# Performance work log

Measured on AMD Instinct MI355X. Metric: run time of the kernel, lower is better.

## Reference

```python
import jax, jax.numpy as jnp
import numpy as np

N, E, F, H, L, G, O = 100000, 1600000, 128, 128, 4, 512, 10
BN_EPS = 1e-5


def setup_inputs() -> dict:
    key = jax.random.key(0)
    ks = jax.random.split(key, 12)
    x = jax.random.normal(ks[0], (N, F), dtype=jnp.float32)
    edge_index = jax.random.randint(ks[1], (2, E), 0, N, dtype=jnp.int32)
    batch = jnp.sort(jax.random.randint(ks[2], (N,), 0, G, dtype=jnp.int32))
    s = 1.0 / np.sqrt(H)
    # 4 GIN layers, input_dim == hidden_dim so params stack uniformly
    W1s = jax.random.uniform(ks[3], (L, F, H), jnp.float32, -s, s)
    b1s = jnp.zeros((L, H), jnp.float32)
    W2s = jax.random.uniform(ks[4], (L, H, H), jnp.float32, -s, s)
    b2s = jnp.zeros((L, H), jnp.float32)
    eps = jnp.zeros((L,), jnp.float32)  # learnable eps, init 0
    gammas = jnp.ones((L, H), jnp.float32)
    betas = jnp.zeros((L, H), jnp.float32)
    Din = F + L * H  # concatenated graph embedding dim
    so = 1.0 / np.sqrt(Din)
    Wout = jax.random.uniform(ks[5], (Din, O), jnp.float32, -so, so)
    bout = jnp.zeros((O,), jnp.float32)
    return {"x": x, "edge_index": edge_index, "batch": batch,
            "W1s": W1s, "b1s": b1s, "W2s": W2s, "b2s": b2s, "eps": eps,
            "gammas": gammas, "betas": betas, "Wout": Wout, "bout": bout}


def reference(x, edge_index, batch, W1s, b1s, W2s, b2s, eps, gammas, betas, Wout, bout):
    src, dst = edge_index[0], edge_index[1]
    n = x.shape[0]
    pooled = [jax.ops.segment_sum(x, batch, num_segments=G)]  # [G, F]
    h = x
    for l in range(W1s.shape[0]):
        # GINConv: MLP((1+eps)*h + sum_{j in N(i)} h_j)
        agg = jax.ops.segment_sum(h[src], dst, num_segments=n)  # [N, H]
        z = (1.0 + eps[l]) * h + agg
        z = jax.nn.relu(z @ W1s[l] + b1s[l]) @ W2s[l] + b2s[l]
        # BatchNorm1d (batch statistics, biased variance) + ReLU; dropout=identity (eval)
        mu = z.mean(axis=0)
        var = z.var(axis=0)
        z = (z - mu) * jax.lax.rsqrt(var + BN_EPS) * gammas[l] + betas[l]
        h = jax.nn.relu(z)
        pooled.append(jax.ops.segment_sum(h, batch, num_segments=G))  # [G, H]
    emb = jnp.concatenate(pooled, axis=1)  # [G, F + L*H]
    return emb @ Wout + bout  # [G, O]
```

## Files before the change

### kernel.cpp

```cpp
#include <hip/hip_runtime.h>
#include <hip/hip_bf16.h>

typedef __attribute__((ext_vector_type(8))) __bf16 bf16x8;
typedef __attribute__((ext_vector_type(4))) float f32x4;
typedef unsigned short u16;
typedef unsigned int u32;

constexpr int Nn = 100000;
constexpr int Ee = 1600000;
constexpr int Hd = 128;
constexpr int Ll = 4;
constexpr int Gg = 512;
constexpr int Oo = 10;
constexpr int Din = Hd + Ll * Hd;
constexpr int SPLIT = 8;
constexpr int NBLK = (Nn + 127) / 128;

constexpr int NB = 256;
constexpr int NPB = 392;
constexpr int BCAP = 8192;
constexpr int BATCH = 8192;
constexpr int NBATCH = (Ee + BATCH - 1) / BATCH;

__device__ __forceinline__ int swzb(int row, int bc) {
  return (row << 8) + (bc ^ ((row & 7) << 4));
}

__device__ __forceinline__ u16 f2bf(float f) {
  __hip_bfloat16 b = __float2bfloat16(f);
  u16 u;
  __builtin_memcpy(&u, &b, 2);
  return u;
}

__device__ __forceinline__ float bf2f(u32 u) { return __uint_as_float(u << 16); }

__device__ __forceinline__ int lower_bound_dev(const int* a, int n, int key) {
  int lo = 0, hi = n;
  while (lo < hi) { int mid = (lo + hi) >> 1; if (a[mid] < key) lo = mid + 1; else hi = mid; }
  return lo;
}

__global__ __launch_bounds__(256) void xcvt_kernel(const float* __restrict__ x, __hip_bfloat16* __restrict__ xb) {
  int i = blockIdx.x * 256 + threadIdx.x;
  const int total = Nn * Hd / 8;
  if (i >= total) return;
  f32x4 v0 = *(const f32x4*)(x + (size_t)i * 8);
  f32x4 v1 = *(const f32x4*)(x + (size_t)i * 8 + 4);
  uint4 o;
  o.x = (u32)f2bf(v0[0]) | ((u32)f2bf(v0[1]) << 16);
  o.y = (u32)f2bf(v0[2]) | ((u32)f2bf(v0[3]) << 16);
  o.z = (u32)f2bf(v1[0]) | ((u32)f2bf(v1[1]) << 16);
  o.w = (u32)f2bf(v1[2]) | ((u32)f2bf(v1[3]) << 16);
  *(uint4*)((u16*)xb + (size_t)i * 8) = o;
}

__global__ __launch_bounds__(256) void wprep_kernel(const float* __restrict__ W1s,
                                                    const float* __restrict__ W2s,
                                                    __hip_bfloat16* __restrict__ wt) {
  int idx = blockIdx.x * 256 + threadIdx.x;
  if (idx >= Ll * 2 * Hd * Hd) return;
  int l = idx >> 15;
  int w = (idx >> 14) & 1;
  int nn = (idx >> 7) & 127;
  int k = idx & 127;
  const float* W = w ? W2s : W1s;
  wt[idx] = __float2bfloat16(W[l * Hd * Hd + k * Hd + nn]);
}

__global__ void initgptr_kernel(int* __restrict__ gptr) {
  int i = threadIdx.x;
  if (i < NB) gptr[i] = i * BCAP;
}

__global__ __launch_bounds__(256) void binA_kernel(const int* __restrict__ src, const int* __restrict__ dst,
                                                   int* __restrict__ gptr, u32* __restrict__ buckets) {
  __shared__ int hist[NB];
  __shared__ int lbase[NB];
  __shared__ int lpos[NB];
  __shared__ int gbaseS[NB];
  __shared__ int scanT[NB];
  __shared__ u32 reorder[BATCH];
  const int tid = threadIdx.x;
  const int e0 = blockIdx.x * BATCH;
  const int n = min(BATCH, Ee - e0);

  hist[tid] = 0;
  __syncthreads();
  for (int k = tid; k < n; k += 256) {
    int d = dst[e0 + k];
    atomicAdd(&hist[d / NPB], 1);
  }
  __syncthreads();
  int v = hist[tid];
  scanT[tid] = v;
  __syncthreads();
  for (int off = 1; off < NB; off <<= 1) {
    int x = (tid >= off) ? scanT[tid - off] : 0;
    __syncthreads();
    scanT[tid] += x;
    __syncthreads();
  }
  lbase[tid] = scanT[tid] - v;
  lpos[tid] = 0;
  __syncthreads();
  for (int k = tid; k < n; k += 256) {
    int d = dst[e0 + k];
    int s = src[e0 + k];
    int b = d / NPB;
    int dlo = d - b * NPB;
    int p = lbase[b] + atomicAdd(&lpos[b], 1);
    reorder[p] = ((u32)dlo << 17) | (u32)s;
  }
  __syncthreads();
  if (hist[tid] > 0) gbaseS[tid] = atomicAdd(&gptr[tid], hist[tid]);
  __syncthreads();
  for (int p = tid; p < n; p += 256) {
    int lo = 0, hi = NB - 1;
    while (lo < hi) { int mid = (lo + hi + 1) >> 1; if (lbase[mid] <= p) lo = mid; else hi = mid - 1; }
    buckets[gbaseS[lo] + (p - lbase[lo])] = reorder[p];
  }
}

__global__ __launch_bounds__(256) void bucketscan_kernel(const int* __restrict__ gptr,
                                                         int* __restrict__ bmeta,
                                                         int* __restrict__ indptr) {
  __shared__ int sc[NB];
  int tid = threadIdx.x;
  int cnt = gptr[tid] - tid * BCAP;
  sc[tid] = cnt;
  __syncthreads();
  for (int off = 1; off < NB; off <<= 1) {
    int x = (tid >= off) ? sc[tid - off] : 0;
    __syncthreads();
    sc[tid] += x;
    __syncthreads();
  }
  bmeta[tid] = cnt;
  bmeta[NB + tid] = sc[tid] - cnt;
  if (tid == 0) indptr[Nn] = Ee;
}

__global__ __launch_bounds__(512) void place_kernel(const u32* __restrict__ buckets,
                                                    const int* __restrict__ bmeta,
                                                    int* __restrict__ indptr, int* __restrict__ adj) {
  __shared__ int ncnt[512];
  __shared__ int nofs[NPB];
  __shared__ int lcur[NPB];
  const int tid = threadIdx.x;
  const int b = blockIdx.x;
  const int cnt = bmeta[b];
  const int adjbase = bmeta[NB + b];
  const int ebase = b * BCAP;
  const int node0 = b * NPB;
  const int nnodes = min(NPB, Nn - node0);

  ncnt[tid] = 0;
  if (tid < NPB) lcur[tid] = 0;
  __syncthreads();
  for (int k = tid; k < cnt; k += 512) atomicAdd(&ncnt[buckets[ebase + k] >> 17], 1);
  __syncthreads();
  int v = ncnt[tid];
  for (int off = 1; off < 512; off <<= 1) {
    int x = (tid >= off) ? ncnt[tid - off] : 0;
    __syncthreads();
    ncnt[tid] += x;
    __syncthreads();
  }
  if (tid < NPB) nofs[tid] = ncnt[tid] - v;
  __syncthreads();
  if (tid < nnodes) indptr[node0 + tid] = adjbase + nofs[tid];
  for (int k = tid; k < cnt; k += 512) {
    u32 u = buckets[ebase + k];
    int dlo = u >> 17;
    int s = (int)(u & 0x1FFFFu);
    int p = atomicAdd(&lcur[dlo], 1);
    adj[adjbase + nofs[dlo] + p] = s;
  }
}

__global__ __launch_bounds__(256) void agg_kernel(const __hip_bfloat16* __restrict__ hb,
                                                  const int* __restrict__ indptr,
                                                  const int* __restrict__ adj,
                                                  const float* __restrict__ epsp,
                                                  int layer, __hip_bfloat16* __restrict__ t) {
  int wid = blockIdx.x * 4 + (threadIdx.x >> 6);
  if (wid >= Nn) return;
  int lane = threadIdx.x & 63;
  int cb = lane * 2;
  const u16* hp = (const u16*)hb;
  u32 selfu = *(const u32*)(hp + (size_t)wid * Hd + cb);
  float eps1 = 1.0f + epsp[layer];
  int s = __builtin_amdgcn_readfirstlane(indptr[wid]);
  int e = __builtin_amdgcn_readfirstlane(indptr[wid + 1]);
  float a0 = 0.f, a1 = 0.f;
  int p = s;
  while (p + 16 <= e) {
    u32 v[16];
    #pragma unroll
    for (int j = 0; j < 16; ++j) v[j] = *(const u32*)(hp + (size_t)adj[p + j] * Hd + cb);
    #pragma unroll
    for (int j = 0; j < 16; ++j) { a0 += bf2f(v[j] & 0xffffu); a1 += bf2f(v[j] >> 16); }
    p += 16;
  }
  if (p + 8 <= e) {
    u32 v[8];
    #pragma unroll
    for (int j = 0; j < 8; ++j) v[j] = *(const u32*)(hp + (size_t)adj[p + j] * Hd + cb);
    #pragma unroll
    for (int j = 0; j < 8; ++j) { a0 += bf2f(v[j] & 0xffffu); a1 += bf2f(v[j] >> 16); }
    p += 8;
  }
  if (p + 4 <= e) {
    u32 v[4];
    #pragma unroll
    for (int j = 0; j < 4; ++j) v[j] = *(const u32*)(hp + (size_t)adj[p + j] * Hd + cb);
    #pragma unroll
    for (int j = 0; j < 4; ++j) { a0 += bf2f(v[j] & 0xffffu); a1 += bf2f(v[j] >> 16); }
    p += 4;
  }
  for (; p < e; ++p) {
    u32 v0 = *(const u32*)(hp + (size_t)adj[p] * Hd + cb);
    a0 += bf2f(v0 & 0xffffu);
    a1 += bf2f(v0 >> 16);
  }
  a0 += eps1 * bf2f(selfu & 0xffffu);
  a1 += eps1 * bf2f(selfu >> 16);
  u32 outv = (u32)f2bf(a0) | ((u32)f2bf(a1) << 16);
  *(u32*)((u16*)t + (size_t)wid * Hd + cb) = outv;
}

__global__ __launch_bounds__(256) void mlp_kernel(const __hip_bfloat16* __restrict__ t,
                                                  const __hip_bfloat16* __restrict__ w1t,
                                                  const __hip_bfloat16* __restrict__ w2t,
                                                  const float* __restrict__ b1,
                                                  const float* __restrict__ b2,
                                                  __hip_bfloat16* __restrict__ z,
                                                  float* __restrict__ pstats) {
  __shared__ __align__(16) unsigned char sA[32 * 1024];
  __shared__ __align__(16) unsigned char sW[32 * 1024];
  const int tid = threadIdx.x;
  const int m0 = blockIdx.x * 128;

  for (int c = tid; c < 2048; c += 256) {
    int row = c >> 4, bc = (c & 15) << 4;
    int so = swzb(row, bc);
    *(uint4*)(sW + so) = *(const uint4*)((const unsigned char*)w1t + row * 256 + bc);
    uint4 av = make_uint4(0u, 0u, 0u, 0u);
    int gr = m0 + row;
    if (gr < Nn) av = *(const uint4*)((const unsigned char*)t + (size_t)gr * 256 + bc);
    *(uint4*)(sA + so) = av;
  }
  __syncthreads();

  const int lane = tid & 63;
  const int wave = tid >> 6;
  const int lrow = lane & 15;
  const int lkb = (lane >> 4) << 4;
  const int wm = wave * 32;
  const int crow = (lane >> 4) << 2;

  f32x4 acc[2][8];
  #pragma unroll
  for (int a = 0; a < 2; ++a) {
    #pragma unroll
    for (int b = 0; b < 8; ++b) acc[a][b] = (f32x4){0.f, 0.f, 0.f, 0.f};
  }

  #pragma unroll
  for (int kk = 0; kk < 4; ++kk) {
    const int kb2 = kk * 64 + lkb;
    bf16x8 a0 = *(const bf16x8*)(sA + swzb(wm + lrow, kb2));
    bf16x8 a1 = *(const bf16x8*)(sA + swzb(wm + 16 + lrow, kb2));
    #pragma unroll
    for (int nf = 0; nf < 8; ++nf) {
      bf16x8 bfr = *(const bf16x8*)(sW + swzb(nf * 16 + lrow, kb2));
      acc[0][nf] = __builtin_amdgcn_mfma_f32_16x16x32_bf16(a0, bfr, acc[0][nf], 0, 0, 0);
      acc[1][nf] = __builtin_amdgcn_mfma_f32_16x16x32_bf16(a1, bfr, acc[1][nf], 0, 0, 0);
    }
  }
  __syncthreads();

  for (int c = tid; c < 2048; c += 256) {
    int row = c >> 4, bc = (c & 15) << 4;
    *(uint4*)(sW + swzb(row, bc)) = *(const uint4*)((const unsigned char*)w2t + row * 256 + bc);
  }
  #pragma unroll
  for (int nf = 0; nf < 8; ++nf) {
    const int col = nf * 16 + lrow;
    const float bb = b1[col];
    #pragma unroll
    for (int mf = 0; mf < 2; ++mf) {
      #pragma unroll
      for (int j = 0; j < 4; ++j) {
        float v = acc[mf][nf][j] + bb;
        v = v > 0.f ? v : 0.f;
        int row = wm + mf * 16 + crow + j;
        *(u16*)(sA + swzb(row, col * 2)) = f2bf(v);
      }
    }
  }
  __syncthreads();

  f32x4 acc2[2][8];
  #pragma unroll
  for (int a = 0; a < 2; ++a) {
    #pragma unroll
    for (int b = 0; b < 8; ++b) acc2[a][b] = (f32x4){0.f, 0.f, 0.f, 0.f};
  }
  #pragma unroll
  for (int kk = 0; kk < 4; ++kk) {
    const int kb2 = kk * 64 + lkb;
    bf16x8 a0 = *(const bf16x8*)(sA + swzb(wm + lrow, kb2));
    bf16x8 a1 = *(const bf16x8*)(sA + swzb(wm + 16 + lrow, kb2));
    #pragma unroll
    for (int nf = 0; nf < 8; ++nf) {
      bf16x8 bfr = *(const bf16x8*)(sW + swzb(nf * 16 + lrow, kb2));
      acc2[0][nf] = __builtin_amdgcn_mfma_f32_16x16x32_bf16(a0, bfr, acc2[0][nf], 0, 0, 0);
      acc2[1][nf] = __builtin_amdgcn_mfma_f32_16x16x32_bf16(a1, bfr, acc2[1][nf], 0, 0, 0);
    }
  }
  __syncthreads();

  float* sred = (float*)sA;
  float* qred = (float*)(sA + 2048);
  u16* zp = (u16*)z;
  #pragma unroll
  for (int nf = 0; nf < 8; ++nf) {
    const int col = nf * 16 + lrow;
    const float bb = b2[col];
    float s = 0.f, q = 0.f;
    #pragma unroll
    for (int mf = 0; mf < 2; ++mf) {
      #pragma unroll
      for (int j = 0; j < 4; ++j) {
        int grow = m0 + wm + mf * 16 + crow + j;
        if (grow < Nn) {
          float v = acc2[mf][nf][j] + bb;
          zp[(size_t)grow * Hd + col] = f2bf(v);
          s += v; q += v * v;
        }
      }
    }
    s += __shfl_xor(s, 16, 64); s += __shfl_xor(s, 32, 64);
    q += __shfl_xor(q, 16, 64); q += __shfl_xor(q, 32, 64);
    if (lane < 16) { sred[wave * 128 + col] = s; qred[wave * 128 + col] = q; }
  }
  __syncthreads();
  if (tid < 128) {
    float a = sred[tid] + sred[128 + tid] + sred[256 + tid] + sred[384 + tid];
    pstats[(size_t)blockIdx.x * 256 + tid] = a;
  } else {
    int c = tid - 128;
    float a = qred[c] + qred[128 + c] + qred[256 + c] + qred[384 + c];
    pstats[(size_t)blockIdx.x * 256 + tid] = a;
  }
}

__global__ __launch_bounds__(256) void stats_bn_kernel(const float* __restrict__ pstats,
                                                       const float* __restrict__ gammas,
                                                       const float* __restrict__ betas,
                                                       int layer, float* __restrict__ ss) {
  __shared__ float reds[256];
  __shared__ float redq[256];
  int f = blockIdx.x;
  int t = threadIdx.x;
  float s = 0.f, q = 0.f;
  for (int i = t; i < NBLK; i += 256) {
    s += pstats[(size_t)i * 256 + f];
    q += pstats[(size_t)i * 256 + 128 + f];
  }
  reds[t] = s; redq[t] = q;
  __syncthreads();
  for (int o = 128; o > 0; o >>= 1) {
    if (t < o) { reds[t] += reds[t + o]; redq[t] += redq[t + o]; }
    __syncthreads();
  }
  if (t == 0) {
    const float invn = 1.0f / (float)Nn;
    float mu = reds[0] * invn;
    float var = redq[0] * invn - mu * mu;
    float sc = gammas[layer * Hd + f] * rsqrtf(var + 1e-5f);
    ss[f] = sc;
    ss[Hd + f] = betas[layer * Hd + f] - mu * sc;
  }
}

__global__ __launch_bounds__(128) void pool_kernel(const __hip_bfloat16* __restrict__ v,
                                                   const int* __restrict__ batch,
                                                   float* __restrict__ emb, int colOff) {
  int g = blockIdx.x / SPLIT, sp = blockIdx.x % SPLIT;
  int c2 = (threadIdx.x & 63) * 2;
  int rh = threadIdx.x >> 6;
  int lo = lower_bound_dev(batch, Nn, g);
  int hi = lower_bound_dev(batch, Nn, g + 1);
  int len = hi - lo;
  if (len <= 0) return;
  int chunk = (len + SPLIT - 1) / SPLIT;
  int rs = lo + sp * chunk;
  int re = min(rs + chunk, hi);
  if (rs >= re) return;
  const u16* vp = (const u16*)v;
  float a0 = 0.f, a1 = 0.f;
  for (int i = rs + rh; i < re; i += 2) {
    u32 u = *(const u32*)(vp + (size_t)i * Hd + c2);
    a0 += bf2f(u & 0xffffu);
    a1 += bf2f(u >> 16);
  }
  atomicAdd(&emb[g * Din + colOff + c2], a0);
  atomicAdd(&emb[g * Din + colOff + c2 + 1], a1);
}

__global__ __launch_bounds__(128) void bn_pool_kernel(const __hip_bfloat16* __restrict__ z,
                                                      const float* __restrict__ ss,
                                                      const int* __restrict__ batch,
                                                      __hip_bfloat16* __restrict__ h,
                                                      float* __restrict__ emb, int colOff) {
  int g = blockIdx.x / SPLIT, sp = blockIdx.x % SPLIT;
  int c2 = (threadIdx.x & 63) * 2;
  int rh = threadIdx.x >> 6;
  float sc0 = ss[c2], sh0 = ss[Hd + c2];
  float sc1 = ss[c2 + 1], sh1 = ss[Hd + c2 + 1];
  int lo = lower_bound_dev(batch, Nn, g);
  int hi = lower_bound_dev(batch, Nn, g + 1);
  int len = hi - lo;
  if (len <= 0) return;
  int chunk = (len + SPLIT - 1) / SPLIT;
  int rs = lo + sp * chunk;
  int re = min(rs + chunk, hi);
  if (rs >= re) return;
  const u16* zp = (const u16*)z;
  u16* hp = (u16*)h;
  float a0 = 0.f, a1 = 0.f;
  for (int i = rs + rh; i < re; i += 2) {
    u32 v = *(const u32*)(zp + (size_t)i * Hd + c2);
    float v0 = bf2f(v & 0xffffu) * sc0 + sh0; v0 = fmaxf(v0, 0.f);
    float v1 = bf2f(v >> 16) * sc1 + sh1; v1 = fmaxf(v1, 0.f);
    *(u32*)(hp + (size_t)i * Hd + c2) = (u32)f2bf(v0) | ((u32)f2bf(v1) << 16);
    a0 += v0; a1 += v1;
  }
  atomicAdd(&emb[g * Din + colOff + c2], a0);
  atomicAdd(&emb[g * Din + colOff + c2 + 1], a1);
}

__global__ __launch_bounds__(64) void out_kernel(const float* __restrict__ emb, const float* __restrict__ Wout,
                                                 const float* __restrict__ bout, float* __restrict__ out) {
  int g = blockIdx.x;
  int lane = threadIdx.x;
  float acc[Oo];
  #pragma unroll
  for (int o = 0; o < Oo; ++o) acc[o] = 0.f;
  for (int d = lane; d < Din; d += 64) {
    float ev = emb[g * Din + d];
    #pragma unroll
    for (int o = 0; o < Oo; ++o) acc[o] += ev * Wout[d * Oo + o];
  }
  #pragma unroll
  for (int off = 32; off > 0; off >>= 1) {
    #pragma unroll
    for (int o = 0; o < Oo; ++o) acc[o] += __shfl_down(acc[o], off, 64);
  }
  if (lane == 0) {
    #pragma unroll
    for (int o = 0; o < Oo; ++o) out[g * Oo + o] = acc[o] + bout[o];
  }
}

extern "C" void kernel_launch(void* const* d_in, const int* in_sizes, int n_in,
                              void* d_out, int out_size, void* d_ws, size_t ws_size,
                              hipStream_t stream) {
  (void)in_sizes; (void)n_in; (void)out_size;
  const float* x = (const float*)d_in[0];
  const int* ei = (const int*)d_in[1];
  const int* src = ei;
  const int* dst = ei + Ee;
  const int* batch = (const int*)d_in[2];
  const float* W1s = (const float*)d_in[3];
  const float* b1s = (const float*)d_in[4];
  const float* W2s = (const float*)d_in[5];
  const float* b2s = (const float*)d_in[6];
  const float* eps = (const float*)d_in[7];
  const float* gammas = (const float*)d_in[8];
  const float* betas = (const float*)d_in[9];
  const float* Wout = (const float*)d_in[10];
  const float* bout = (const float*)d_in[11];
  float* out = (float*)d_out;

  unsigned char* ws = (unsigned char*)d_ws;
  size_t off = 0;
  auto alloc = [&](size_t bytes) -> void* {
    void* p = ws + off;
    off = (off + bytes + 255) & ~size_t(255);
    return p;
  };
  __hip_bfloat16* xb = (__hip_bfloat16*)alloc((size_t)Nn * Hd * 2);
  __hip_bfloat16* h = (__hip_bfloat16*)alloc((size_t)Nn * Hd * 2);
  __hip_bfloat16* z = (__hip_bfloat16*)alloc((size_t)Nn * Hd * 2);
  __hip_bfloat16* t = (__hip_bfloat16*)alloc((size_t)Nn * Hd * 2);
  int* indptr = (int*)alloc((size_t)(Nn + 1) * 4);
  int* adj = (int*)alloc((size_t)Ee * 4);
  u32* buckets = (u32*)alloc((size_t)NB * BCAP * 4);
  int* gptr = (int*)alloc((size_t)NB * 4);
  int* bmeta = (int*)alloc((size_t)2 * NB * 4);
  float* emb = (float*)alloc((size_t)Gg * Din * 4);
  float* pstats = (float*)alloc((size_t)NBLK * 256 * 4);
  float* ss = (float*)alloc(256 * 4);
  __hip_bfloat16* wt = (__hip_bfloat16*)alloc((size_t)Ll * 2 * Hd * Hd * 2);
  if (off > ws_size) return;

  hipMemsetAsync(emb, 0, (size_t)Gg * Din * 4, stream);

  xcvt_kernel<<<(Nn * Hd / 8 + 255) / 256, 256, 0, stream>>>(x, xb);
  wprep_kernel<<<(Ll * 2 * Hd * Hd + 255) / 256, 256, 0, stream>>>(W1s, W2s, wt);

  initgptr_kernel<<<1, NB, 0, stream>>>(gptr);
  binA_kernel<<<NBATCH, 256, 0, stream>>>(src, dst, gptr, buckets);
  bucketscan_kernel<<<1, NB, 0, stream>>>(gptr, bmeta, indptr);
  place_kernel<<<NB, 512, 0, stream>>>(buckets, bmeta, indptr, adj);

  pool_kernel<<<Gg * SPLIT, 128, 0, stream>>>(xb, batch, emb, 0);

  const __hip_bfloat16* hcur = xb;
  for (int l = 0; l < Ll; ++l) {
    agg_kernel<<<(Nn + 3) / 4, 256, 0, stream>>>(hcur, indptr, adj, eps, l, t);
    mlp_kernel<<<NBLK, 256, 0, stream>>>(
        t, wt + (size_t)l * 2 * Hd * Hd, wt + (size_t)l * 2 * Hd * Hd + Hd * Hd,
        b1s + l * Hd, b2s + l * Hd, z, pstats);
    stats_bn_kernel<<<128, 256, 0, stream>>>(pstats, gammas, betas, l, ss);
    bn_pool_kernel<<<Gg * SPLIT, 128, 0, stream>>>(z, ss, batch, h, emb, Hd + l * Hd);
    hcur = h;
  }

  out_kernel<<<Gg, 64, 0, stream>>>(emb, Wout, bout, out);
}
```

Baseline: 592.4 us.

## Fuse neighbor aggregation into MLP kernel and apply BN-ReLU lazily on gather

Neighbor aggregation now runs inside the MLP kernel: each block gathers its 128 nodes' neighbor sums straight into shared memory, so the intermediate t buffer is no longer written and re-read. The previous layer's BatchNorm scale/shift and ReLU are applied on the fly to raw z values during the gather, so bn_pool no longer has to write h back to memory. In exchange the affine+max is recomputed for every edge rather than once per node. Aggregation occupancy also changes, since each wave now handles 32 nodes in sequence inside a block that holds 64KB of LDS.

```diff
diff --git a/kernel.cpp b/kernel.cpp
--- a/kernel.cpp
+++ b/kernel.cpp
@@ -66,6 +66,12 @@
   int k = idx & 127;
   const float* W = w ? W2s : W1s;
   wt[idx] = __float2bfloat16(W[l * Hd * Hd + k * Hd + nn]);
+}
+
+__global__ void initss_kernel(float* __restrict__ ss) {
+  int f = threadIdx.x;
+  ss[f] = 1.f;
+  ss[Hd + f] = 0.f;
 }
 
 __global__ void initgptr_kernel(int* __restrict__ gptr) {
@@ -179,82 +185,94 @@
   }
 }
 
-__global__ __launch_bounds__(256) void agg_kernel(const __hip_bfloat16* __restrict__ hb,
-                                                  const int* __restrict__ indptr,
-                                                  const int* __restrict__ adj,
-                                                  const float* __restrict__ epsp,
-                                                  int layer, __hip_bfloat16* __restrict__ t) {
-  int wid = blockIdx.x * 4 + (threadIdx.x >> 6);
-  if (wid >= Nn) return;
-  int lane = threadIdx.x & 63;
-  int cb = lane * 2;
-  const u16* hp = (const u16*)hb;
-  u32 selfu = *(const u32*)(hp + (size_t)wid * Hd + cb);
-  float eps1 = 1.0f + epsp[layer];
-  int s = __builtin_amdgcn_readfirstlane(indptr[wid]);
-  int e = __builtin_amdgcn_readfirstlane(indptr[wid + 1]);
-  float a0 = 0.f, a1 = 0.f;
-  int p = s;
-  while (p + 16 <= e) {
-    u32 v[16];
-    #pragma unroll
-    for (int j = 0; j < 16; ++j) v[j] = *(const u32*)(hp + (size_t)adj[p + j] * Hd + cb);
-    #pragma unroll
-    for (int j = 0; j < 16; ++j) { a0 += bf2f(v[j] & 0xffffu); a1 += bf2f(v[j] >> 16); }
-    p += 16;
-  }
-  if (p + 8 <= e) {
-    u32 v[8];
-    #pragma unroll
-    for (int j = 0; j < 8; ++j) v[j] = *(const u32*)(hp + (size_t)adj[p + j] * Hd + cb);
-    #pragma unroll
-    for (int j = 0; j < 8; ++j) { a0 += bf2f(v[j] & 0xffffu); a1 += bf2f(v[j] >> 16); }
-    p += 8;
-  }
-  if (p + 4 <= e) {
-    u32 v[4];
-    #pragma unroll
-    for (int j = 0; j < 4; ++j) v[j] = *(const u32*)(hp + (size_t)adj[p + j] * Hd + cb);
-    #pragma unroll
-    for (int j = 0; j < 4; ++j) { a0 += bf2f(v[j] & 0xffffu); a1 += bf2f(v[j] >> 16); }
-    p += 4;
-  }
-  for (; p < e; ++p) {
-    u32 v0 = *(const u32*)(hp + (size_t)adj[p] * Hd + cb);
-    a0 += bf2f(v0 & 0xffffu);
-    a1 += bf2f(v0 >> 16);
-  }
-  a0 += eps1 * bf2f(selfu & 0xffffu);
-  a1 += eps1 * bf2f(selfu >> 16);
-  u32 outv = (u32)f2bf(a0) | ((u32)f2bf(a1) << 16);
-  *(u32*)((u16*)t + (size_t)wid * Hd + cb) = outv;
-}
-
-__global__ __launch_bounds__(256) void mlp_kernel(const __hip_bfloat16* __restrict__ t,
-                                                  const __hip_bfloat16* __restrict__ w1t,
-                                                  const __hip_bfloat16* __restrict__ w2t,
-                                                  const float* __restrict__ b1,
-                                                  const float* __restrict__ b2,
-                                                  __hip_bfloat16* __restrict__ z,
-                                                  float* __restrict__ pstats) {
+__global__ __launch_bounds__(256) void fused_kernel(const __hip_bfloat16* __restrict__ zprev,
+                                                    const int* __restrict__ indptr,
+                                                    const int* __restrict__ adj,
+                                                    const float* __restrict__ ssin,
+                                                    const float* __restrict__ epsp, int layer, float negLim,
+                                                    const __hip_bfloat16* __restrict__ w1t,
+                                                    const __hip_bfloat16* __restrict__ w2t,
+                                                    const float* __restrict__ b1,
+                                                    const float* __restrict__ b2,
+                                                    __hip_bfloat16* __restrict__ zout,
+                                                    float* __restrict__ pstats) {
   __shared__ __align__(16) unsigned char sA[32 * 1024];
   __shared__ __align__(16) unsigned char sW[32 * 1024];
   const int tid = threadIdx.x;
   const int m0 = blockIdx.x * 128;
+  const int lane = tid & 63;
+  const int wave = tid >> 6;
 
   for (int c = tid; c < 2048; c += 256) {
     int row = c >> 4, bc = (c & 15) << 4;
-    int so = swzb(row, bc);
-    *(uint4*)(sW + so) = *(const uint4*)((const unsigned char*)w1t + row * 256 + bc);
-    uint4 av = make_uint4(0u, 0u, 0u, 0u);
-    int gr = m0 + row;
-    if (gr < Nn) av = *(const uint4*)((const unsigned char*)t + (size_t)gr * 256 + bc);
-    *(uint4*)(sA + so) = av;
-  }
-  __syncthreads();
-
-  const int lane = tid & 63;
-  const int wave = tid >> 6;
+    *(uint4*)(sW + swzb(row, bc)) = *(const uint4*)((const unsigned char*)w1t + row * 256 + bc);
+  }
+
+  {
+    const int cb = lane * 2;
+    const u16* zp = (const u16*)zprev;
+    const float sc0 = ssin[cb], sh0 = ssin[Hd + cb];
+    const float sc1 = ssin[cb + 1], sh1 = ssin[Hd + cb + 1];
+    const float eps1 = 1.0f + epsp[layer];
+    for (int nd = 0; nd < 32; ++nd) {
+      const int row = wave * 32 + nd;
+      const int node = m0 + row;
+      u32 val = 0u;
+      if (node < Nn) {
+        int s = __builtin_amdgcn_readfirstlane(indptr[node]);
+        int e = __builtin_amdgcn_readfirstlane(indptr[node + 1]);
+        float a0 = 0.f, a1 = 0.f;
+        int p = s;
+        while (p + 16 <= e) {
+          u32 v[16];
+          #pragma unroll
+          for (int j = 0; j < 16; ++j) v[j] = *(const u32*)(zp + (size_t)adj[p + j] * Hd + cb);
+          #pragma unroll
+          for (int j = 0; j < 16; ++j) {
+            a0 += fmaxf(fmaf(bf2f(v[j] & 0xffffu), sc0, sh0), negLim);
+            a1 += fmaxf(fmaf(bf2f(v[j] >> 16), sc1, sh1), negLim);
+          }
+          p += 16;
+        }
+        if (p + 8 <= e) {
+          u32 v[8];
+          #pragma unroll
+          for (int j = 0; j < 8; ++j) v[j] = *(const u32*)(zp + (size_t)adj[p + j] * Hd + cb);
+          #pragma unroll
+          for (int j = 0; j < 8; ++j) {
+            a0 += fmaxf(fmaf(bf2f(v[j] & 0xffffu), sc0, sh0), negLim);
+            a1 += fmaxf(fmaf(bf2f(v[j] >> 16), sc1, sh1), negLim);
+          }
+          p += 8;
+        }
+        if (p + 4 <= e) {
+          u32 v[4];
+          #pragma unroll
+          for (int j = 0; j < 4; ++j) v[j] = *(const u32*)(zp + (size_t)adj[p + j] * Hd + cb);
+          #pragma unroll
+          for (int j = 0; j < 4; ++j) {
+            a0 += fmaxf(fmaf(bf2f(v[j] & 0xffffu), sc0, sh0), negLim);
+            a1 += fmaxf(fmaf(bf2f(v[j] >> 16), sc1, sh1), negLim);
+          }
+          p += 4;
+        }
+        for (; p < e; ++p) {
+          u32 v0 = *(const u32*)(zp + (size_t)adj[p] * Hd + cb);
+          a0 += fmaxf(fmaf(bf2f(v0 & 0xffffu), sc0, sh0), negLim);
+          a1 += fmaxf(fmaf(bf2f(v0 >> 16), sc1, sh1), negLim);
+        }
+        u32 sv = *(const u32*)(zp + (size_t)node * Hd + cb);
+        float s0 = fmaxf(fmaf(bf2f(sv & 0xffffu), sc0, sh0), negLim);
+        float s1 = fmaxf(fmaf(bf2f(sv >> 16), sc1, sh1), negLim);
+        float t0 = eps1 * s0 + a0;
+        float t1 = eps1 * s1 + a1;
+        val = (u32)f2bf(t0) | ((u32)f2bf(t1) << 16);
+      }
+      *(u32*)(sA + swzb(row, lane * 4)) = val;
+    }
+  }
+  __syncthreads();
+
   const int lrow = lane & 15;
   const int lkb = (lane >> 4) << 4;
   const int wm = wave * 32;
@@ -324,7 +342,7 @@
 
   float* sred = (float*)sA;
   float* qred = (float*)(sA + 2048);
-  u16* zp = (u16*)z;
+  u16* zp2 = (u16*)zout;
   #pragma unroll
   for (int nf = 0; nf < 8; ++nf) {
     const int col = nf * 16 + lrow;
@@ -337,7 +355,7 @@
         int grow = m0 + wm + mf * 16 + crow + j;
         if (grow < Nn) {
           float v = acc2[mf][nf][j] + bb;
-          zp[(size_t)grow * Hd + col] = f2bf(v);
+          zp2[(size_t)grow * Hd + col] = f2bf(v);
           s += v; q += v * v;
         }
       }
@@ -411,11 +429,10 @@
   atomicAdd(&emb[g * Din + colOff + c2 + 1], a1);
 }
 
-__global__ __launch_bounds__(128) void bn_pool_kernel(const __hip_bfloat16* __restrict__ z,
-                                                      const float* __restrict__ ss,
-                                                      const int* __restrict__ batch,
-                                                      __hip_bfloat16* __restrict__ h,
-                                                      float* __restrict__ emb, int colOff) {
+__global__ __launch_bounds__(128) void pool_z_kernel(const __hip_bfloat16* __restrict__ z,
+                                                     const float* __restrict__ ss,
+                                                     const int* __restrict__ batch,
+                                                     float* __restrict__ emb, int colOff) {
   int g = blockIdx.x / SPLIT, sp = blockIdx.x % SPLIT;
   int c2 = (threadIdx.x & 63) * 2;
   int rh = threadIdx.x >> 6;
@@ -430,14 +447,11 @@
   int re = min(rs + chunk, hi);
   if (rs >= re) return;
   const u16* zp = (const u16*)z;
-  u16* hp = (u16*)h;
   float a0 = 0.f, a1 = 0.f;
   for (int i = rs + rh; i < re; i += 2) {
     u32 v = *(const u32*)(zp + (size_t)i * Hd + c2);
-    float v0 = bf2f(v & 0xffffu) * sc0 + sh0; v0 = fmaxf(v0, 0.f);
-    float v1 = bf2f(v >> 16) * sc1 + sh1; v1 = fmaxf(v1, 0.f);
-    *(u32*)(hp + (size_t)i * Hd + c2) = (u32)f2bf(v0) | ((u32)f2bf(v1) << 16);
-    a0 += v0; a1 += v1;
+    a0 += fmaxf(fmaf(bf2f(v & 0xffffu), sc0, sh0), 0.f);
+    a1 += fmaxf(fmaf(bf2f(v >> 16), sc1, sh1), 0.f);
   }
   atomicAdd(&emb[g * Din + colOff + c2], a0);
   atomicAdd(&emb[g * Din + colOff + c2 + 1], a1);
@@ -494,9 +508,8 @@
     return p;
   };
   __hip_bfloat16* xb = (__hip_bfloat16*)alloc((size_t)Nn * Hd * 2);
-  __hip_bfloat16* h = (__hip_bfloat16*)alloc((size_t)Nn * Hd * 2);
-  __hip_bfloat16* z = (__hip_bfloat16*)alloc((size_t)Nn * Hd * 2);
-  __hip_bfloat16* t = (__hip_bfloat16*)alloc((size_t)Nn * Hd * 2);
+  __hip_bfloat16* zA = (__hip_bfloat16*)alloc((size_t)Nn * Hd * 2);
+  __hip_bfloat16* zB = (__hip_bfloat16*)alloc((size_t)Nn * Hd * 2);
   int* indptr = (int*)alloc((size_t)(Nn + 1) * 4);
   int* adj = (int*)alloc((size_t)Ee * 4);
   u32* buckets = (u32*)alloc((size_t)NB * BCAP * 4);
@@ -504,7 +517,7 @@
   int* bmeta = (int*)alloc((size_t)2 * NB * 4);
   float* emb = (float*)alloc((size_t)Gg * Din * 4);
   float* pstats = (float*)alloc((size_t)NBLK * 256 * 4);
-  float* ss = (float*)alloc(256 * 4);
+  float* ssbuf = (float*)alloc((size_t)(Ll + 1) * 256 * 4);
   __hip_bfloat16* wt = (__hip_bfloat16*)alloc((size_t)Ll * 2 * Hd * Hd * 2);
   if (off > ws_size) return;
 
@@ -512,6 +525,7 @@
 
   xcvt_kernel<<<(Nn * Hd / 8 + 255) / 256, 256, 0, stream>>>(x, xb);
   wprep_kernel<<<(Ll * 2 * Hd * Hd + 255) / 256, 256, 0, stream>>>(W1s, W2s, wt);
+  initss_kernel<<<1, 128, 0, stream>>>(ssbuf);
 
   initgptr_kernel<<<1, NB, 0, stream>>>(gptr);
   binA_kernel<<<NBATCH, 256, 0, stream>>>(src, dst, gptr, buckets);
@@ -520,15 +534,17 @@
 
   pool_kernel<<<Gg * SPLIT, 128, 0, stream>>>(xb, batch, emb, 0);
 
-  const __hip_bfloat16* hcur = xb;
+  const __hip_bfloat16* zprev = xb;
   for (int l = 0; l < Ll; ++l) {
-    agg_kernel<<<(Nn + 3) / 4, 256, 0, stream>>>(hcur, indptr, adj, eps, l, t);
-    mlp_kernel<<<NBLK, 256, 0, stream>>>(
-        t, wt + (size_t)l * 2 * Hd * Hd, wt + (size_t)l * 2 * Hd * Hd + Hd * Hd,
-        b1s + l * Hd, b2s + l * Hd, z, pstats);
-    stats_bn_kernel<<<128, 256, 0, stream>>>(pstats, gammas, betas, l, ss);
-    bn_pool_kernel<<<Gg * SPLIT, 128, 0, stream>>>(z, ss, batch, h, emb, Hd + l * Hd);
-    hcur = h;
+    __hip_bfloat16* zcur = (l & 1) ? zB : zA;
+    float negLim = (l == 0) ? -3.4e38f : 0.f;
+    fused_kernel<<<NBLK, 256, 0, stream>>>(
+        zprev, indptr, adj, ssbuf + (size_t)l * 256, eps, l, negLim,
+        wt + (size_t)l * 2 * Hd * Hd, wt + (size_t)l * 2 * Hd * Hd + Hd * Hd,
+        b1s + l * Hd, b2s + l * Hd, zcur, pstats);
+    stats_bn_kernel<<<128, 256, 0, stream>>>(pstats, gammas, betas, l, ssbuf + (size_t)(l + 1) * 256);
+    pool_z_kernel<<<Gg * SPLIT, 128, 0, stream>>>(zcur, ssbuf + (size_t)(l + 1) * 256, batch, emb, Hd + l * Hd);
+    zprev = zcur;
   }
 
   out_kernel<<<Gg, 64, 0, stream>>>(emb, Wout, bout, out);
```

Result: slower. 898.3 us (+51.6%).
